# Performance work log

Hardware: AMD Instinct MI355X
Metric: run time of the kernel (lower is better)

The kernel has to match this reference:

```python
import jax, jax.numpy as jnp
import numpy as np
import math

B, S, D, H = 2, 2048, 1024, 16
HD = D // H  # head dim = 64


def _rope_tables():
    # RoFormer sinusoidal position embedding: one frequency per (even, odd) pair
    pos = jnp.arange(S, dtype=jnp.float32)[:, None]                # [S, 1]
    inv_freq = 1.0 / (10000.0 ** (jnp.arange(0, HD, 2, dtype=jnp.float32) / HD))  # [HD/2]
    ang = pos * inv_freq[None, :]                                   # [S, HD/2]
    sin = jnp.sin(ang)[None, None]                                  # [1,1,S,HD/2]
    cos = jnp.cos(ang)[None, None]
    return sin, cos


def setup_inputs() -> dict:
    key = jax.random.key(0)
    k0, k1, k2, k3 = jax.random.split(key, 4)
    scale = 1.0 / math.sqrt(D)
    sin, cos = _rope_tables()
    return {
        "hidden_states": jax.random.normal(k0, (B, S, D), dtype=jnp.float32),
        "Wq": jax.random.normal(k1, (D, D), dtype=jnp.float32) * scale,
        "Wk": jax.random.normal(k2, (D, D), dtype=jnp.float32) * scale,
        "Wv": jax.random.normal(k3, (D, D), dtype=jnp.float32) * scale,
        "sin": sin,
        "cos": cos,
    }


def _split_heads(x):
    # [B,S,D] -> [B,H,S,HD]
    b, s, _ = x.shape
    return x.reshape(b, s, H, HD).transpose(0, 2, 1, 3)


def _apply_rotary(x, sin, cos):
    # x: [B,H,S,HD]; sin/cos broadcast as [1,1,S,HD/2]
    x1 = x[..., 0::2]
    x2 = x[..., 1::2]
    out = jnp.stack([x1 * cos - x2 * sin, x2 * cos + x1 * sin], axis=-1)
    return out.reshape(x.shape)


def reference(hidden_states, Wq, Wk, Wv, sin, cos):
    q = _apply_rotary(_split_heads(hidden_states @ Wq), sin, cos)  # [B,H,S,HD]
    k = _apply_rotary(_split_heads(hidden_states @ Wk), sin, cos)
    v = _apply_rotary(_split_heads(hidden_states @ Wv), sin, cos)  # note: RoPE on V too, per source
    scores = jnp.einsum("bhqd,bhkd->bhqk", q, k) / math.sqrt(HD)   # [B,H,S,S]
    probs = jax.nn.softmax(scores, axis=-1)
    ctx = jnp.einsum("bhqk,bhkd->bhqd", probs, v)                   # [B,H,S,HD]
    return ctx.transpose(0, 2, 1, 3).reshape(hidden_states.shape[0], S, D)
```

## Files before the change

### kernel.cpp

```cpp
#include <hip/hip_runtime.h>

typedef unsigned short u16;
typedef unsigned short u16x8 __attribute__((ext_vector_type(8)));
typedef unsigned short u16x4 __attribute__((ext_vector_type(4)));
typedef short s16x4 __attribute__((ext_vector_type(4)));
typedef __bf16 bf16x8_t __attribute__((ext_vector_type(8)));
typedef float floatx4 __attribute__((ext_vector_type(4)));

#define BATCH 2
#define S_LEN 2048
#define D_DIM 1024
#define NH    16
#define HD    64

__device__ __forceinline__ u16 f2b(float f) {
  union { float f; unsigned int i; } c; c.f = f;
  const unsigned int i = c.i;
  return (u16)((i + 0x7FFFu + ((i >> 16) & 1u)) >> 16);
}
__device__ __forceinline__ unsigned int fbits(float f) {
  union { float f; unsigned int i; } c; c.f = f; return c.i;
}
__device__ __forceinline__ bf16x8_t asbf(u16x8 v) {
  union { u16x8 u; bf16x8_t b; } c; c.u = v; return c.b;
}
__device__ __forceinline__ s16x4 as4(uint2 v) {
  union { uint2 u; s16x4 s; } c; c.u = v; return c.s;
}
__device__ __forceinline__ s16x4 as4u(u16x4 v) {
  union { u16x4 u; s16x4 s; } c; c.u = v; return c.s;
}
__device__ __forceinline__ void load_lds16(const u16* g, u16* l) {
  __builtin_amdgcn_global_load_lds(
      (const __attribute__((address_space(1))) void*)g,
      (__attribute__((address_space(3))) void*)l, 16, 0, 0);
}

__device__ __attribute__((aligned(256))) u16 g_xb[(size_t)BATCH * S_LEN * D_DIM];
__device__ __attribute__((aligned(256))) u16 g_wt[3u * D_DIM * D_DIM];
__device__ __attribute__((aligned(256))) u16 g_qkv[3u * BATCH * S_LEN * D_DIM];

__global__ __launch_bounds__(256) void prep(const float* __restrict__ X,
                                            const float* __restrict__ Wq,
                                            const float* __restrict__ Wk,
                                            const float* __restrict__ Wv) {
  const int tid = threadIdx.x;
  const int z = blockIdx.y;
  if (z == 3) {
#pragma unroll
    for (int c = 0; c < 8; ++c) {
      const size_t i = (((size_t)c * 256 + blockIdx.x) * 256 + tid) * 8;
      floatx4 a = *(const floatx4*)(X + i);
      floatx4 b = *(const floatx4*)(X + i + 4);
      u16x8 o;
#pragma unroll
      for (int j = 0; j < 4; ++j) { o[j] = f2b(a[j]); o[4 + j] = f2b(b[j]); }
      *(u16x8*)(g_xb + i) = o;
    }
    return;
  }
  __shared__ u16 t[64][65];
  const float* W = (z == 0) ? Wq : (z == 1) ? Wk : Wv;
  u16* Wt = g_wt + (size_t)z * D_DIM * D_DIM;
  const int k0 = (blockIdx.x & 15) * 64;
  const int n0 = (blockIdx.x >> 4) * 64;
  const int rr = tid >> 4;
  const int cc = (tid & 15) * 4;
#pragma unroll
  for (int i = 0; i < 4; ++i) {
    const int r = rr + i * 16;
    floatx4 v = *(const floatx4*)(W + (size_t)(k0 + r) * D_DIM + n0 + cc);
    t[r][cc] = f2b(v[0]); t[r][cc + 1] = f2b(v[1]);
    t[r][cc + 2] = f2b(v[2]); t[r][cc + 3] = f2b(v[3]);
  }
  __syncthreads();
#pragma unroll
  for (int i = 0; i < 4; ++i) {
    const int r = rr + i * 16;
    u16x4 v;
    v[0] = t[cc][r]; v[1] = t[cc + 1][r]; v[2] = t[cc + 2][r]; v[3] = t[cc + 3][r];
    *(u16x4*)(Wt + (size_t)(n0 + r) * D_DIM + k0 + cc) = v;
  }
}

__global__ __launch_bounds__(256) void qkv_gemm(const float* __restrict__ sin_t,
                                                const float* __restrict__ cos_t) {
  __shared__ __attribute__((aligned(16))) u16 lds_a[128 * 32];
  __shared__ __attribute__((aligned(16))) u16 lds_b[128 * 32];
  const int tid = threadIdx.x;
  const int wv = tid >> 6;
  const int lane = tid & 63;
  const int lrow = lane & 15;
  const int quad = lane >> 4;
  const int wr = wv >> 1, wc = wv & 1;
  const int m0 = blockIdx.x * 128;
  const int n0 = blockIdx.y * 128;
  const int z = blockIdx.z;
  const bool vmode = (z == 2);
  const u16* Wz = g_wt + (size_t)z * (D_DIM * D_DIM);

  floatx4 acc[4][4] = {};

  const u16* gA = g_xb + (size_t)(m0 + wv * 32 + (lane >> 2)) * D_DIM + (lane & 3) * 8;
  const u16* gB = Wz   + (size_t)(n0 + wv * 32 + (lane >> 2)) * D_DIM + (lane & 3) * 8;
  u16* sA = &lds_a[(wv * 32) * 32];
  u16* sB = &lds_b[(wv * 32) * 32];

  const u16* Aarr = vmode ? lds_a : lds_b;
  const u16* Barr = vmode ? lds_b : lds_a;

  for (int k0 = 0; k0 < D_DIM; k0 += 32) {
    __syncthreads();
    load_lds16(gA + k0, sA);
    load_lds16(gA + (size_t)16 * D_DIM + k0, sA + 512);
    load_lds16(gB + k0, sB);
    load_lds16(gB + (size_t)16 * D_DIM + k0, sB + 512);
    __syncthreads();
    u16x8 af[4], bfr[4];
#pragma unroll
    for (int mi = 0; mi < 4; ++mi)
      af[mi] = *(const u16x8*)&Aarr[(wr * 64 + mi * 16 + lrow) * 32 + quad * 8];
#pragma unroll
    for (int ni = 0; ni < 4; ++ni)
      bfr[ni] = *(const u16x8*)&Barr[(wc * 64 + ni * 16 + lrow) * 32 + quad * 8];
#pragma unroll
    for (int mi = 0; mi < 4; ++mi)
#pragma unroll
      for (int ni = 0; ni < 4; ++ni)
        acc[mi][ni] = __builtin_amdgcn_mfma_f32_16x16x32_bf16(
            asbf(af[mi]), asbf(bfr[ni]), acc[mi][ni], 0, 0, 0);
  }

  if (!vmode) {
    const float qsc = (z == 0) ? 0.18033688011112042f : 1.0f;
    u16* outz = g_qkv + (size_t)z * (BATCH * S_LEN * D_DIM);
#pragma unroll
    for (int mi = 0; mi < 4; ++mi) {
      const int nf0 = n0 + wr * 64 + mi * 16 + quad * 4;
      const int h = nf0 >> 6, hd0 = nf0 & 63, i00 = hd0 >> 1;
#pragma unroll
      for (int ni = 0; ni < 4; ++ni) {
        const int sg = m0 + wc * 64 + ni * 16 + lrow;
        const int b = sg >> 11, srow = sg & 2047;
        const float c0 = cos_t[(size_t)srow * 32 + i00];
        const float s0 = sin_t[(size_t)srow * 32 + i00];
        const float c1 = cos_t[(size_t)srow * 32 + i00 + 1];
        const float s1 = sin_t[(size_t)srow * 32 + i00 + 1];
        const float v0 = acc[mi][ni][0], v1 = acc[mi][ni][1];
        const float v2 = acc[mi][ni][2], v3 = acc[mi][ni][3];
        u16x4 ov;
        ov[0] = f2b((v0 * c0 - v1 * s0) * qsc);
        ov[1] = f2b((v1 * c0 + v0 * s0) * qsc);
        ov[2] = f2b((v2 * c1 - v3 * s1) * qsc);
        ov[3] = f2b((v3 * c1 + v2 * s1) * qsc);
        *(u16x4*)(outz + ((size_t)(b * NH + h) * S_LEN + srow) * HD + hd0) = ov;
      }
    }
  } else {
    u16* outv = g_qkv + (size_t)2 * (BATCH * S_LEN * D_DIM);
#pragma unroll
    for (int mi = 0; mi < 4; ++mi) {
      const int s0g = m0 + wr * 64 + mi * 16 + quad * 4;
      const int b = s0g >> 11, sl = s0g & 2047;
#pragma unroll
      for (int ni = 0; ni < 4; ++ni) {
        const int nf = n0 + wc * 64 + ni * 16 + lrow;
        const int h = nf >> 6, hd = nf & 63, i0 = hd >> 1;
        const float sgn = (hd & 1) ? 1.f : -1.f;
        u16x4 ov;
#pragma unroll
        for (int r = 0; r < 4; ++r) {
          const int s = sl + r;
          const float c  = cos_t[(size_t)s * 32 + i0];
          const float sn = sin_t[(size_t)s * 32 + i0];
          const float v  = acc[mi][ni][r];
          const float vp = __shfl_xor(v, 1);
          ov[r] = f2b(v * c + sgn * sn * vp);
        }
        *(u16x4*)(outv + (size_t)(b * NH + h) * (S_LEN * HD) +
                  ((size_t)(sl >> 2) * HD + hd) * 4) = ov;
      }
    }
  }
}

__global__ __launch_bounds__(256) void flash_attn(float* __restrict__ out) {
  __shared__ float red[64 * 65];
  __shared__ float lred[4 * 64];
  const int bh = blockIdx.x;
  const int qt = blockIdx.y;
  const int b = bh >> 4, h = bh & 15;
  const int tid = threadIdx.x, wv = tid >> 6, lane = tid & 63;
  const int lrow = lane & 15, quad = lane >> 4;
  const u16* Qb  = g_qkv + (size_t)bh * (S_LEN * HD);
  const u16* Kb  = g_qkv + (size_t)(BATCH * NH + bh) * (S_LEN * HD);
  const u16* VTb = g_qkv + (size_t)(2 * BATCH * NH + bh) * (S_LEN * HD);
  const int qbase = qt * 64;

  u16x8 qf[4][2];
#pragma unroll
  for (int nb = 0; nb < 4; ++nb)
#pragma unroll
    for (int ks = 0; ks < 2; ++ks)
      qf[nb][ks] = *(const u16x8*)(Qb + (size_t)(qbase + nb * 16 + lrow) * HD +
                                   ks * 32 + quad * 8);

  floatx4 oacc[4][4] = {};
  float lacc[4] = {};

  const u16* Kw = Kb + (size_t)(wv * 16 + lrow) * HD + quad * 8;
  const u16* Vw = VTb + ((size_t)(wv * 4 + quad) * HD + lrow) * 4;

  auto loadK = [&](u16x8* kr, int t) {
    const u16* p = Kw + (size_t)t * 64 * HD;
    kr[0] = *(const u16x8*)(p);
    kr[1] = *(const u16x8*)(p + 32);
  };
  auto loadV = [&](u16x4* vr, int t) {
    const u16* p = Vw + (size_t)t * 16 * HD * 4;
#pragma unroll
    for (int hb = 0; hb < 4; ++hb)
      vr[hb] = *(const u16x4*)(p + hb * 16 * 4);
  };
  auto tile = [&](const u16x8* kr, const u16x4* vr) {
    floatx4 sacc[4];
    __builtin_amdgcn_s_setprio(1);
#pragma unroll
    for (int nb = 0; nb < 4; ++nb) {
      floatx4 s0 = {};
      s0 = __builtin_amdgcn_mfma_f32_16x16x32_bf16(asbf(kr[0]), asbf(qf[nb][0]), s0, 0, 0, 0);
      sacc[nb] = __builtin_amdgcn_mfma_f32_16x16x32_bf16(asbf(kr[1]), asbf(qf[nb][1]), s0, 0, 0, 0);
    }
    __builtin_amdgcn_s_setprio(0);
    s16x4 pa[4];
#pragma unroll
    for (int nb = 0; nb < 4; ++nb) {
      const float p0 = __builtin_amdgcn_exp2f(sacc[nb][0]);
      const float p1 = __builtin_amdgcn_exp2f(sacc[nb][1]);
      const float p2 = __builtin_amdgcn_exp2f(sacc[nb][2]);
      const float p3 = __builtin_amdgcn_exp2f(sacc[nb][3]);
      lacc[nb] += (p0 + p1) + (p2 + p3);
      uint2 pk;
      pk.x = __byte_perm(fbits(p0), fbits(p1), 0x7632);
      pk.y = __byte_perm(fbits(p2), fbits(p3), 0x7632);
      pa[nb] = as4(pk);
    }
    __builtin_amdgcn_s_setprio(1);
#pragma unroll
    for (int nb = 0; nb < 4; ++nb)
#pragma unroll
      for (int hb = 0; hb < 4; ++hb)
        oacc[nb][hb] = __builtin_amdgcn_mfma_f32_16x16x16bf16_1k(
            pa[nb], as4u(vr[hb]), oacc[nb][hb], 0, 0, 0);
    __builtin_amdgcn_s_setprio(0);
  };

  u16x8 kA[2], kB[2];
  u16x4 vA[4], vB[4];
  loadK(kA, 0); loadV(vA, 0);
  for (int t = 0; t < S_LEN / 64; t += 2) {
    loadK(kB, t + 1); loadV(vB, t + 1);
    tile(kA, vA);
    if (t + 2 < S_LEN / 64) { loadK(kA, t + 2); loadV(vA, t + 2); }
    tile(kB, vB);
  }

  float lw[4];
#pragma unroll
  for (int nb = 0; nb < 4; ++nb) {
    float l = lacc[nb];
    l += __shfl_xor(l, 16);
    l += __shfl_xor(l, 32);
    lw[nb] = l;
  }
  if (quad == 0) {
#pragma unroll
    for (int nb = 0; nb < 4; ++nb) lred[wv * 64 + nb * 16 + lrow] = lw[nb];
  }
  for (int ph = 0; ph < 4; ++ph) {
    if (wv == ph) {
#pragma unroll
      for (int nb = 0; nb < 4; ++nb)
#pragma unroll
        for (int hb = 0; hb < 4; ++hb) {
          const int hd = hb * 16 + lrow;
#pragma unroll
          for (int r = 0; r < 4; ++r) {
            const int q = nb * 16 + quad * 4 + r;
            if (ph == 0) red[q * 65 + hd] = oacc[nb][hb][r];
            else         red[q * 65 + hd] += oacc[nb][hb][r];
          }
        }
    }
    __syncthreads();
  }
#pragma unroll
  for (int p = 0; p < 16; ++p) {
    const int q = wv * 16 + p;
    const float lt = lred[q] + lred[64 + q] + lred[128 + q] + lred[192 + q];
    const float o = red[q * 65 + lane] * (1.f / lt);
    out[((size_t)(b * S_LEN) + qbase + q) * D_DIM + h * HD + lane] = o;
  }
}

extern "C" void kernel_launch(void* const* d_in, const int* in_sizes, int n_in,
                              void* d_out, int out_size, void* d_ws, size_t ws_size,
                              hipStream_t stream) {
  const float* X = (const float*)d_in[0];
  const float* sin_t = (const float*)d_in[4];
  const float* cos_t = (const float*)d_in[5];

  prep<<<dim3(256, 4), 256, 0, stream>>>(X, (const float*)d_in[1],
                                         (const float*)d_in[2],
                                         (const float*)d_in[3]);

  qkv_gemm<<<dim3(32, 8, 3), 256, 0, stream>>>(sin_t, cos_t);

  flash_attn<<<dim3(32, 32), 256, 0, stream>>>((float*)d_out);
}
```

Before: 193.7 us.

## Stage K/V tiles through double-buffered LDS with cooperative coalesced global loads

Each wave used to load its own K and V fragments straight from global memory into registers, with a two-tile register ping-pong. Now all 256 threads cooperatively load each 64-key K/V tile with contiguous 16-byte loads into a double-buffered, padded LDS area. Loads for the next tile are issued during the current tile's work, and each wave reads its MFMA fragments from LDS. This aims for better global coalescing, but it adds a __syncthreads per tile plus extra LDS write/read traffic. The reduction buffers are now aliased onto the K/V LDS arrays.

```diff
diff --git a/kernel.cpp b/kernel.cpp
--- a/kernel.cpp
+++ b/kernel.cpp
@@ -184,17 +184,18 @@
   }
 }
 
+#define VP 260
 __global__ __launch_bounds__(256) void flash_attn(float* __restrict__ out) {
-  __shared__ float red[64 * 65];
-  __shared__ float lred[4 * 64];
+  __shared__ __attribute__((aligned(16))) u16 lds_k[2][64 * 72];
+  __shared__ __attribute__((aligned(16))) u16 lds_v[2][16 * VP];
   const int bh = blockIdx.x;
   const int qt = blockIdx.y;
   const int b = bh >> 4, h = bh & 15;
   const int tid = threadIdx.x, wv = tid >> 6, lane = tid & 63;
   const int lrow = lane & 15, quad = lane >> 4;
-  const u16* Qb  = g_qkv + (size_t)bh * (S_LEN * HD);
-  const u16* Kb  = g_qkv + (size_t)(BATCH * NH + bh) * (S_LEN * HD);
-  const u16* VTb = g_qkv + (size_t)(2 * BATCH * NH + bh) * (S_LEN * HD);
+  const u16* Qb = g_qkv + (size_t)bh * (S_LEN * HD);
+  const u16* Kb = g_qkv + (size_t)(BATCH * NH + bh) * (S_LEN * HD);
+  const u16* Vb = g_qkv + (size_t)(2 * BATCH * NH + bh) * (S_LEN * HD);
   const int qbase = qt * 64;
 
   u16x8 qf[4][2];
@@ -208,30 +209,61 @@
   floatx4 oacc[4][4] = {};
   float lacc[4] = {};
 
-  const u16* Kw = Kb + (size_t)(wv * 16 + lrow) * HD + quad * 8;
-  const u16* Vw = VTb + ((size_t)(wv * 4 + quad) * HD + lrow) * 4;
-
-  auto loadK = [&](u16x8* kr, int t) {
-    const u16* p = Kw + (size_t)t * 64 * HD;
-    kr[0] = *(const u16x8*)(p);
-    kr[1] = *(const u16x8*)(p + 32);
-  };
-  auto loadV = [&](u16x4* vr, int t) {
-    const u16* p = Vw + (size_t)t * 16 * HD * 4;
+  const int sr = tid >> 3;
+  const int sc = (tid & 7) * 8;
+
+  u16x8 kreg[2], vreg[2];
+#pragma unroll
+  for (int i = 0; i < 2; ++i)
+    kreg[i] = *(const u16x8*)(Kb + (size_t)(sr + i * 32) * HD + sc);
+#pragma unroll
+  for (int c = 0; c < 2; ++c)
+    vreg[c] = *(const u16x8*)(Vb + (size_t)c * 2048 + tid * 8);
+
+  for (int t = 0; t < S_LEN / 64; ++t) {
+    const int buf = t & 1;
+#pragma unroll
+    for (int i = 0; i < 2; ++i)
+      *(u16x8*)&lds_k[buf][(sr + i * 32) * 72 + sc] = kreg[i];
+#pragma unroll
+    for (int c = 0; c < 2; ++c) {
+      const int off = c * 2048 + tid * 8;
+      *(u16x8*)&lds_v[buf][(off >> 8) * VP + (off & 255)] = vreg[c];
+    }
+    __syncthreads();
+    if (t + 1 < S_LEN / 64) {
+      const size_t kn = (size_t)(t + 1) * 64 * HD;
+#pragma unroll
+      for (int i = 0; i < 2; ++i)
+        kreg[i] = *(const u16x8*)(Kb + kn + (size_t)(sr + i * 32) * HD + sc);
+#pragma unroll
+      for (int c = 0; c < 2; ++c)
+        vreg[c] = *(const u16x8*)(Vb + kn + (size_t)c * 2048 + tid * 8);
+    }
+
+    u16x8 kf[2];
+#pragma unroll
+    for (int ks = 0; ks < 2; ++ks)
+      kf[ks] = *(const u16x8*)&lds_k[buf][(wv * 16 + lrow) * 72 +
+                                          ks * 32 + quad * 8];
+    u16x4 vf[4];
 #pragma unroll
     for (int hb = 0; hb < 4; ++hb)
-      vr[hb] = *(const u16x4*)(p + hb * 16 * 4);
-  };
-  auto tile = [&](const u16x8* kr, const u16x4* vr) {
+      vf[hb] = *(const u16x4*)&lds_v[buf][(wv * 4 + quad) * VP +
+                                          (hb * 16 + lrow) * 4];
+
     floatx4 sacc[4];
     __builtin_amdgcn_s_setprio(1);
 #pragma unroll
     for (int nb = 0; nb < 4; ++nb) {
       floatx4 s0 = {};
-      s0 = __builtin_amdgcn_mfma_f32_16x16x32_bf16(asbf(kr[0]), asbf(qf[nb][0]), s0, 0, 0, 0);
-      sacc[nb] = __builtin_amdgcn_mfma_f32_16x16x32_bf16(asbf(kr[1]), asbf(qf[nb][1]), s0, 0, 0, 0);
+      s0 = __builtin_amdgcn_mfma_f32_16x16x32_bf16(
+          asbf(kf[0]), asbf(qf[nb][0]), s0, 0, 0, 0);
+      sacc[nb] = __builtin_amdgcn_mfma_f32_16x16x32_bf16(
+          asbf(kf[1]), asbf(qf[nb][1]), s0, 0, 0, 0);
     }
     __builtin_amdgcn_s_setprio(0);
+
     s16x4 pa[4];
 #pragma unroll
     for (int nb = 0; nb < 4; ++nb) {
@@ -245,25 +277,21 @@
       pk.y = __byte_perm(fbits(p2), fbits(p3), 0x7632);
       pa[nb] = as4(pk);
     }
+
     __builtin_amdgcn_s_setprio(1);
 #pragma unroll
     for (int nb = 0; nb < 4; ++nb)
 #pragma unroll
       for (int hb = 0; hb < 4; ++hb)
         oacc[nb][hb] = __builtin_amdgcn_mfma_f32_16x16x16bf16_1k(
-            pa[nb], as4u(vr[hb]), oacc[nb][hb], 0, 0, 0);
+            pa[nb], as4u(vf[hb]), oacc[nb][hb], 0, 0, 0);
     __builtin_amdgcn_s_setprio(0);
-  };
-
-  u16x8 kA[2], kB[2];
-  u16x4 vA[4], vB[4];
-  loadK(kA, 0); loadV(vA, 0);
-  for (int t = 0; t < S_LEN / 64; t += 2) {
-    loadK(kB, t + 1); loadV(vB, t + 1);
-    tile(kA, vA);
-    if (t + 2 < S_LEN / 64) { loadK(kA, t + 2); loadV(vA, t + 2); }
-    tile(kB, vB);
-  }
+  }
+
+  __syncthreads();
+
+  float* red  = (float*)(&lds_k[0][0]);
+  float* lred = (float*)(&lds_v[0][0]);
 
   float lw[4];
 #pragma unroll
```

New measurement: 196.3 us. About the same (+1.3%).
